# Kernel optimization log

Hardware: AMD Instinct MI355X
Metric: run time of the kernel (lower is better)

Reference implementation:

```python
import jax, jax.numpy as jnp
import numpy as np

# Forest of complete L-ary trees, BFS level-contiguous node numbering.
B_TREES, ARITY, DEPTH = 8, 4, 8
C, M, NGEN = 8, 100, 4
COUNTS = [B_TREES * ARITY**l for l in range(DEPTH + 1)]
OFFS = np.concatenate([[0], np.cumsum(COUNTS)]).astype(np.int64)
DIM = int(OFFS[-1])  # 699048
# tree id of each node: within-level index // (ARITY**level)
BATCH = np.concatenate([np.arange(COUNTS[l]) // (ARITY**l) for l in range(DEPTH + 1)])


def setup_inputs() -> dict:
    key = jax.random.key(0)
    k1, k2, k3, k4 = jax.random.split(key, 4)
    return {
        "x": jax.random.randint(k1, (DIM,), 0, M, dtype=jnp.int32),
        "A": jax.random.normal(k2, (C, C, ARITY, NGEN), dtype=jnp.float32) * 2.5,
        "B_emit": jax.random.normal(k3, (C, M, NGEN), dtype=jnp.float32) * 2.5,
        "Pi": jax.random.normal(k4, (C, NGEN), dtype=jnp.float32) * 2.5,
    }


def _htmm_loglik(x, A, B_emit, Pi):
    # softmax reparameterization (matches F.softmax axes in torch code)
    smA = jax.nn.softmax(A, axis=0)            # [C,C,L,G], over child state
    smA_t = jnp.transpose(smA, (2, 0, 1, 3))   # [L,C,C,G]
    smB = jax.nn.softmax(B_emit, axis=1)       # [C,M,G]
    smPi = jax.nn.softmax(Pi, axis=0)          # [C,G]

    # preliminary downward: prior state distribution per node, level by level.
    # Children of a parent are contiguous with sibling position j = idx % ARITY.
    prior_lvls = [jnp.broadcast_to(smPi, (COUNTS[0], C, NGEN))]
    for l in range(1, DEPTH + 1):
        n_pa = COUNTS[l - 1]
        # prior_child[c] = sum_d A[c, d, pos_j, g] * prior_pa[d]
        pl = jnp.einsum('jcdg,pdg->pjcg', smA_t, prior_lvls[-1])
        prior_lvls.append(pl.reshape(n_pa * ARITY, C, NGEN))
    prior = jnp.concatenate(prior_lvls, axis=0)  # [DIM,C,G]

    em = jnp.transpose(smB[:, x], (1, 0, 2))     # [DIM,C,G]
    beta0 = prior * em

    ll = jnp.zeros((DIM, NGEN), dtype=beta0.dtype)
    # leaves = deepest level
    beta_lvl = beta0[OFFS[DEPTH]:OFFS[DEPTH + 1]]
    nu = beta_lvl.sum(1)                          # [n_leaves,G]
    beta_lvl = beta_lvl / nu[:, None, :]
    ll = ll.at[OFFS[DEPTH]:OFFS[DEPTH + 1]].set(jnp.log(nu))

    # upward recursion, bottom-up
    for l in range(DEPTH, 0, -1):
        n_pa = COUNTS[l - 1]
        ratio = (beta_lvl / prior[OFFS[l]:OFFS[l + 1]]).reshape(n_pa, ARITY, C, NGEN)
        # beta_uv[d] = sum_c A[c, d, pos_j, g] * beta_ch[c] / prior_ch[c]
        beta_uv = jnp.einsum('jcdg,pjcg->pjdg', smA_t, ratio)  # [n_pa,L,C,G]
        beta_pa = beta0[OFFS[l - 1]:OFFS[l]] * jnp.prod(beta_uv, axis=1)
        nu = beta_pa.sum(1)
        beta_lvl = beta_pa / nu[:, None, :]
        ll = ll.at[OFFS[l - 1]:OFFS[l]].set(jnp.log(nu))

    # scatter per-node log-likelihood contributions into per-tree totals
    return jax.ops.segment_sum(ll, jnp.asarray(BATCH), num_segments=B_TREES)  # [B_TREES,G]


def reference(x, A, B_emit, Pi):
    return _htmm_loglik(x, A, B_emit, Pi)
```

## Files before the change

### kernel.cpp

```cpp
#include <hip/hip_runtime.h>

constexpr int OFFS1 = 8, OFFS2 = 40, OFFS3 = 168, OFFS4 = 680;
constexpr int OFFS5 = 2728, OFFS6 = 10920, OFFS7 = 43688, OFFS8 = 174760;


template <int CTRL>
static __device__ __forceinline__ float dppmov(float v) {
  return __int_as_float(__builtin_amdgcn_update_dpp(0, __float_as_int(v), CTRL, 0xF, 0xF, true));
}

static __device__ __forceinline__ float bfly8(float v) {
  v += dppmov<0xB1>(v);
  v += dppmov<0x4E>(v);
  v += dppmov<0x141>(v);
  return v;
}

static __device__ __forceinline__ void oct8(float v, float pv[8]) {
  float m = dppmov<0x141>(v);
  pv[0] = dppmov<0x00>(v); pv[1] = dppmov<0x55>(v);
  pv[2] = dppmov<0xAA>(v); pv[3] = dppmov<0xFF>(v);
  pv[4] = dppmov<0x00>(m); pv[5] = dppmov<0x55>(m);
  pv[6] = dppmov<0xAA>(m); pv[7] = dppmov<0xFF>(m);
}

static __device__ __forceinline__ float dot8(const float w[8], const float v[8]) {
  return w[0]*v[0] + w[1]*v[1] + w[2]*v[2] + w[3]*v[3] +
         w[4]*v[4] + w[5]*v[5] + w[6]*v[6] + w[7]*v[7];
}

static __device__ __forceinline__ void ld8(const float* p, float pv[8]) {
  const float4* q = (const float4*)p;
  float4 a = q[0], b = q[1];
  pv[0] = a.x; pv[1] = a.y; pv[2] = a.z; pv[3] = a.w;
  pv[4] = b.x; pv[5] = b.y; pv[6] = b.z; pv[7] = b.w;
}

static __device__ __forceinline__ void ld8p(const float* p, float wp[8], int h) {
  const float4* q = (const float4*)p;
  float4 a = q[h], b = q[1 - h];
  wp[0] = a.x; wp[1] = a.y; wp[2] = a.z; wp[3] = a.w;
  wp[4] = b.w; wp[5] = b.z; wp[6] = b.y; wp[7] = b.x;
}

static __device__ __forceinline__ float dot8p(const float wp[8], const float* p, int h) {
  const float4* q = (const float4*)p;
  float4 a = q[h], b = q[1 - h];
  return wp[0]*a.x + wp[1]*a.y + wp[2]*a.z + wp[3]*a.w +
         wp[4]*b.w + wp[5]*b.z + wp[6]*b.y + wp[7]*b.x;
}

static __device__ __forceinline__ float rcpf(float x) { return __builtin_amdgcn_rcpf(x); }

static __device__ __forceinline__ float step_down(const float* wtd_l, float v, int j,
                                                  int r, int h) {
  const float* wb = &wtd_l[j * 256 + r];
  float w[8];
#pragma unroll
  for (int k = 0; k < 4; k++) {
    w[k]     = wb[(4 * h + k) * 32];
    w[4 + k] = wb[(7 - 4 * h - k) * 32];
  }
  float pv[8];
  oct8(v, pv);
  return dot8(w, pv);
}

static __device__ __forceinline__ float upprod(const float wup_p[4][8], const float rat[4]) {
  float prod = 1.f;
#pragma unroll
  for (int j = 0; j < 4; j++) {
    float pr[8];
    oct8(rat[j], pr);
    prod *= dot8(wup_p[j], pr);
  }
  return prod;
}

static __device__ __forceinline__ float leaf7(float u7, float e0, float e1, float e2,
                                              float e3, float em, float* acc) {
  float n0 = bfly8(u7 * e0), n1 = bfly8(u7 * e1);
  float n2 = bfly8(u7 * e2), n3 = bfly8(u7 * e3);
  float p01 = n0 * n1, p23 = n2 * n3;
  float prod = (e0 * e1 * rcpf(p01)) * (e2 * e3 * rcpf(p23));
  *acc += __logf(p01) + __logf(p23);
  float nu7 = bfly8(u7 * em * prod);
  *acc += __logf(nu7);
  return em * prod * rcpf(nu7);
}

static __device__ __forceinline__ void build_tables(const float* __restrict__ A,
                                                    const float* __restrict__ Bm,
                                                    const float* __restrict__ Pi,
                                                    float* wtd_l, float* emt_l,
                                                    float* pit_l, float* llb, int t) {
  if (t < 128) {
    int d = t >> 4, j = (t >> 2) & 3, gg = t & 3;
    float v[8], sum = 0.f;
#pragma unroll
    for (int ss = 0; ss < 8; ss++) { v[ss] = __expf(A[((ss * 8 + d) * 4 + j) * 4 + gg]); sum += v[ss]; }
    float inv = rcpf(sum);
#pragma unroll
    for (int ss = 0; ss < 8; ss++) wtd_l[(j * 8 + d) * 32 + gg * 8 + ss] = v[ss] * inv;
  }
  if (t < 4) {
    float v[8], sum = 0.f;
#pragma unroll
    for (int c = 0; c < 8; c++) { v[c] = __expf(Pi[c * 4 + t]); sum += v[c]; }
    float inv = rcpf(sum);
#pragma unroll
    for (int c = 0; c < 8; c++) pit_l[t * 8 + c] = v[c] * inv;
    llb[t] = 0.f;
  }
  {
    int row = t >> 3, part = t & 7, c = row >> 2, gg = row & 3;
    int m0 = part < 4 ? part * 13 : 52 + (part - 4) * 12;
    int mn = part < 4 ? 13 : 12;
    float sum = 0.f;
    for (int m = m0; m < m0 + mn; m++) sum += __expf(Bm[(c * 100 + m) * 4 + gg]);
    sum = bfly8(sum);
    float inv = rcpf(sum);
    for (int m = m0; m < m0 + mn; m++)
      emt_l[m * 32 + gg * 8 + c] = __expf(Bm[(c * 100 + m) * 4 + gg]) * inv;
  }
}

__global__ __launch_bounds__(256) void k_phase1(const int* __restrict__ x,
                                                const float* __restrict__ A,
                                                const float* __restrict__ Bm,
                                                const float* __restrict__ Pi,
                                                float* __restrict__ RAT4,
                                                float* __restrict__ blocksum) {
  __shared__ __align__(16) float wtd_l[1024];
  __shared__ __align__(16) float emt_l[3200];
  __shared__ __align__(16) float pit_l[32];
  __shared__ __align__(16) float rat5buf[16][32];
  __shared__ __align__(16) float pri4buf[4][32];
  __shared__ float llb[4];

  int t = threadIdx.x;
  int r = t & 31, g = r >> 3, s = r & 7, grp = t >> 5;
  int h = s >> 2, gb = g * 8;
  int b = blockIdx.x;

  build_tables(A, Bm, Pi, wtd_l, emt_l, pit_l, llb, t);
  __syncthreads();
  float wtd_p[4][8], wup_p[4][8];
#pragma unroll
  for (int j = 0; j < 4; j++) {
    const float* wb = &wtd_l[j * 256 + r];
#pragma unroll
    for (int k = 0; k < 4; k++) {
      wtd_p[j][k]     = wb[(4 * h + k) * 32];
      wtd_p[j][4 + k] = wb[(7 - 4 * h - k) * 32];
    }
    ld8p(&wtd_l[(j * 8 + s) * 32 + gb], wup_p[j], h);
  }

  float acc = 0.f;
  {
    int n5A = b * 16 + grp, n5B = n5A + 8;
    const int4* x8A = (const int4*)(x + OFFS8 + n5A * 64);
    const int4* x8B = (const int4*)(x + OFFS8 + n5B * 64);
    const int4* x7A = (const int4*)(x + OFFS7 + n5A * 16);
    const int4* x7B = (const int4*)(x + OFFS7 + n5B * 16);
    int4 x6A = *(const int4*)(x + OFFS6 + n5A * 4);
    int4 x6B = *(const int4*)(x + OFFS6 + n5B * 4);
    int x5A = x[OFFS5 + n5A], x5B = x[OFFS5 + n5B];
    const int* x6aA = (const int*)&x6A;
    const int* x6aB = (const int*)&x6B;

    float vA = pit_l[r], vB = vA, pri4A = 0.f, pri4B = 0.f;
#pragma unroll
    for (int k = 1; k <= 5; k++) {
      vA = step_down(wtd_l, vA, (n5A >> (2 * (5 - k))) & 3, r, h);
      vB = step_down(wtd_l, vB, (n5B >> (2 * (5 - k))) & 3, r, h);
      if (k == 4) { pri4A = vA; pri4B = vB; }
    }
    float pv5A[8], pv5B[8];
    oct8(vA, pv5A); oct8(vB, pv5B);

    float rat6A[4], rat6B[4];
#pragma unroll
    for (int q6 = 0; q6 < 4; q6++) {
      float u6A = dot8(wtd_p[q6], pv5A);
      float u6B = dot8(wtd_p[q6], pv5B);
      float pv6A[8], pv6B[8];
      oct8(u6A, pv6A); oct8(u6B, pv6B);
      int4 x7qA = x7A[q6], x7qB = x7B[q6];
      const int* x7aA = (const int*)&x7qA;
      const int* x7aB = (const int*)&x7qB;

      float rat7A[4], rat7B[4];
#pragma unroll
      for (int q7 = 0; q7 < 4; q7++) {
        int4 xlA = x8A[q6 * 4 + q7], xlB = x8B[q6 * 4 + q7];
        const int* xa = (const int*)&xlA;
        const int* xb = (const int*)&xlB;
        float EA[4], EB[4];
#pragma unroll
        for (int j = 0; j < 4; j++) {
          EA[j] = dot8p(wup_p[j], &emt_l[xa[j] * 32 + gb], h);
          EB[j] = dot8p(wup_p[j], &emt_l[xb[j] * 32 + gb], h);
        }
        float u7A = dot8(wtd_p[q7], pv6A);
        float u7B = dot8(wtd_p[q7], pv6B);
        rat7A[q7] = leaf7(u7A, EA[0], EA[1], EA[2], EA[3], emt_l[x7aA[q7] * 32 + r], &acc);
        rat7B[q7] = leaf7(u7B, EB[0], EB[1], EB[2], EB[3], emt_l[x7aB[q7] * 32 + r], &acc);
      }
      float prod6A = upprod(wup_p, rat7A);
      float prod6B = upprod(wup_p, rat7B);
      float em6A = emt_l[x6aA[q6] * 32 + r];
      float em6B = emt_l[x6aB[q6] * 32 + r];
      float nu6A = bfly8(u6A * em6A * prod6A);
      float nu6B = bfly8(u6B * em6B * prod6B);
      acc += __logf(nu6A) + __logf(nu6B);
      rat6A[q6] = em6A * prod6A * rcpf(nu6A);
      rat6B[q6] = em6B * prod6B * rcpf(nu6B);
    }
    float prod5A = upprod(wup_p, rat6A);
    float prod5B = upprod(wup_p, rat6B);
    float em5A = emt_l[x5A * 32 + r], em5B = emt_l[x5B * 32 + r];
    float nu5A = bfly8(vA * em5A * prod5A);
    float nu5B = bfly8(vB * em5B * prod5B);
    acc += __logf(nu5A) + __logf(nu5B);
    rat5buf[grp][r] = em5A * prod5A * rcpf(nu5A);
    rat5buf[8 + grp][r] = em5B * prod5B * rcpf(nu5B);
    if ((grp & 3) == 0) {
      pri4buf[grp >> 2][r] = pri4A;
      pri4buf[2 + (grp >> 2)][r] = pri4B;
    }
  }
  __syncthreads();

  if (grp < 4) {
    int n4 = b * 4 + grp;
    float prod = 1.f;
#pragma unroll
    for (int j = 0; j < 4; j++) prod *= dot8p(wup_p[j], &rat5buf[grp * 4 + j][gb], h);
    float em = emt_l[x[OFFS4 + n4] * 32 + r];
    float pr4 = pri4buf[grp][r];
    float nu = bfly8(pr4 * em * prod);
    acc += __logf(nu);
    RAT4[n4 * 32 + r] = em * prod * rcpf(nu);
  }

  if (s == 0) atomicAdd(&llb[g], acc);
  __syncthreads();
  if (t < 4) blocksum[b * 4 + t] = llb[t];
}

__global__ __launch_bounds__(256) void k_phase2(const int* __restrict__ x,
                                                const float* __restrict__ A,
                                                const float* __restrict__ Bm,
                                                const float* __restrict__ Pi,
                                                const float* __restrict__ RAT4,
                                                const float* __restrict__ blocksum,
                                                float* __restrict__ out) {
  __shared__ __align__(16) float wtd_l[1024];
  __shared__ __align__(16) float emt_l[3200];
  __shared__ __align__(16) float pit_l[32];
  __shared__ __align__(16) float stg[8192];
  __shared__ __align__(16) float xb[640];
  __shared__ float llb[4];

  int t = threadIdx.x;
  int r = t & 31, g = r >> 3, s = r & 7, grp = t >> 5;
  int h = s >> 2, gb = g * 8;
  int tree = blockIdx.x;

  build_tables(A, Bm, Pi, wtd_l, emt_l, pit_l, llb, t);
  {
    const float4* src = (const float4*)(RAT4 + tree * 8192);
    float4* dst = (float4*)stg;
#pragma unroll
    for (int i = 0; i < 8; i++) dst[i * 256 + t] = src[i * 256 + t];
  }
  __syncthreads();

  float wtd_p[4][8], wup_p[4][8];
#pragma unroll
  for (int j = 0; j < 4; j++) {
    const float* wb = &wtd_l[j * 256 + r];
#pragma unroll
    for (int k = 0; k < 4; k++) {
      wtd_p[j][k]     = wb[(4 * h + k) * 32];
      wtd_p[j][4 + k] = wb[(7 - 4 * h - k) * 32];
    }
    ld8p(&wtd_l[(j * 8 + s) * 32 + gb], wup_p[j], h);
  }

  float acc2 = 0.f;
  {
    int n2A = tree * 16 + grp, n2B = n2A + 8;
    int4 x3A = *(const int4*)(x + OFFS3 + n2A * 4);
    int4 x3B = *(const int4*)(x + OFFS3 + n2B * 4);
    int x2A = x[OFFS2 + n2A], x2B = x[OFFS2 + n2B];
    const int* xa = (const int*)&x3A;
    const int* xbv = (const int*)&x3B;
    float v2A = pit_l[r], v2B = v2A;
    v2A = step_down(wtd_l, v2A, (n2A >> 2) & 3, r, h);
    v2B = step_down(wtd_l, v2B, (n2B >> 2) & 3, r, h);
    v2A = step_down(wtd_l, v2A, n2A & 3, r, h);
    v2B = step_down(wtd_l, v2B, n2B & 3, r, h);
    float pv2A[8], pv2B[8];
    oct8(v2A, pv2A); oct8(v2B, pv2B);
    float rat3A[4], rat3B[4];
#pragma unroll
    for (int j3 = 0; j3 < 4; j3++) {
      int i3A = grp * 4 + j3, i3B = (8 + grp) * 4 + j3;
      float p3A = dot8(wtd_p[j3], pv2A);
      float p3B = dot8(wtd_p[j3], pv2B);
      float prodA = 1.f, prodB = 1.f;
#pragma unroll
      for (int j = 0; j < 4; j++) {
        prodA *= dot8p(wup_p[j], &stg[(i3A * 4 + j) * 32 + gb], h);
        prodB *= dot8p(wup_p[j], &stg[(i3B * 4 + j) * 32 + gb], h);
      }
      float emA = emt_l[xa[j3] * 32 + r], emB = emt_l[xbv[j3] * 32 + r];
      float nuA = bfly8(p3A * emA * prodA), nuB = bfly8(p3B * emB * prodB);
      acc2 += __logf(nuA) + __logf(nuB);
      rat3A[j3] = emA * prodA * rcpf(nuA);
      rat3B[j3] = emB * prodB * rcpf(nuB);
    }
    float prodA = upprod(wup_p, rat3A);
    float prodB = upprod(wup_p, rat3B);
    float emA = emt_l[x2A * 32 + r], emB = emt_l[x2B * 32 + r];
    float nuA = bfly8(v2A * emA * prodA), nuB = bfly8(v2B * emB * prodB);
    acc2 += __logf(nuA) + __logf(nuB);
    xb[grp * 32 + r] = emA * prodA * rcpf(nuA);
    xb[(8 + grp) * 32 + r] = emB * prodB * rcpf(nuB);
  }
  __syncthreads();
  if (grp < 4) {
    int n1g = tree * 4 + grp;
    float v1 = step_down(wtd_l, pit_l[r], grp, r, h);
    float prod = 1.f;
#pragma unroll
    for (int j = 0; j < 4; j++) prod *= dot8p(wup_p[j], &xb[(grp * 4 + j) * 32 + gb], h);
    float em = emt_l[x[OFFS1 + n1g] * 32 + r];
    float nu = bfly8(v1 * em * prod);
    acc2 += __logf(nu);
    xb[512 + grp * 32 + r] = em * prod * rcpf(nu);
  }
  __syncthreads();
  if (grp == 0) {
    float pr = pit_l[r];
    float prod = 1.f;
#pragma unroll
    for (int j = 0; j < 4; j++) prod *= dot8p(wup_p[j], &xb[512 + j * 32 + gb], h);
    float em = emt_l[x[tree] * 32 + r];
    float nu = bfly8(pr * em * prod);
    acc2 += __logf(nu);
  }
  __syncthreads();
  if (s == 0) atomicAdd(&llb[g], acc2);
  float v = blocksum[tree * 256 + t];
  __syncthreads();
  stg[t] = v;
  __syncthreads();
#pragma unroll
  for (int off = 128; off >= 4; off >>= 1) {
    if (t < off) stg[t] += stg[t + off];
    __syncthreads();
  }
  if (t < 4) out[tree * 4 + t] = stg[t] + llb[t];
}

extern "C" void kernel_launch(void* const* d_in, const int* in_sizes, int n_in,
                              void* d_out, int out_size, void* d_ws, size_t ws_size,
                              hipStream_t stream) {
  const int* x = (const int*)d_in[0];
  const float* A = (const float*)d_in[1];
  const float* Bm = (const float*)d_in[2];
  const float* Pi = (const float*)d_in[3];
  float* ws = (float*)d_ws;
  float* blocksum = ws + 256;
  float* RAT4 = ws + 256 + 2048;
  float* out = (float*)d_out;

  k_phase1<<<512, 256, 0, stream>>>(x, A, Bm, Pi, RAT4, blocksum);
  k_phase2<<<8, 256, 0, stream>>>(x, A, Bm, Pi, RAT4, blocksum, out);
}
```

Baseline: 94.66 us.

## Halve per-block work, double grid, and use transposed padded down-weights in LDS

Each warp-group now processes one level-5 subtree instead of two, so phase 1 launches twice as many blocks. The per-thread wtd_p register array is dropped; a padded transposed copy of the down-weights (wtdT) is built in LDS and read with float2 loads. Launch bounds request two blocks per CU. The aim is lower register pressure and more waves in flight, paid for by rebuilding the softmax tables in twice as many blocks and by extra LDS reads. Phase 2 now sums two blocksum entries per thread to match the doubled grid.

Result: slower. 100.1 us (+5.8%).

```diff
diff --git a/kernel.cpp b/kernel.cpp
--- a/kernel.cpp
+++ b/kernel.cpp
@@ -29,13 +29,6 @@
          w[4]*v[4] + w[5]*v[5] + w[6]*v[6] + w[7]*v[7];
 }
 
-static __device__ __forceinline__ void ld8(const float* p, float pv[8]) {
-  const float4* q = (const float4*)p;
-  float4 a = q[0], b = q[1];
-  pv[0] = a.x; pv[1] = a.y; pv[2] = a.z; pv[3] = a.w;
-  pv[4] = b.x; pv[5] = b.y; pv[6] = b.z; pv[7] = b.w;
-}
-
 static __device__ __forceinline__ void ld8p(const float* p, float wp[8], int h) {
   const float4* q = (const float4*)p;
   float4 a = q[h], b = q[1 - h];
@@ -50,7 +43,21 @@
          wp[4]*b.w + wp[5]*b.z + wp[6]*b.y + wp[7]*b.x;
 }
 
+static __device__ __forceinline__ float dot8pT(const float wp[8], const float* row, int h) {
+  const float2* q = (const float2*)row;
+  float2 a = q[2 * h], b = q[2 * h + 1], c = q[3 - 2 * h], d = q[2 - 2 * h];
+  return wp[0]*a.x + wp[1]*a.y + wp[2]*b.x + wp[3]*b.y +
+         wp[4]*c.y + wp[5]*c.x + wp[6]*d.y + wp[7]*d.x;
+}
+
 static __device__ __forceinline__ float rcpf(float x) { return __builtin_amdgcn_rcpf(x); }
+
+static __device__ __forceinline__ float step_downT(const float* wtdT, float v, int j,
+                                                   int sg, int h) {
+  float pv[8];
+  oct8(v, pv);
+  return dot8pT(pv, &wtdT[(j * 32 + sg) * 10], h);
+}
 
 static __device__ __forceinline__ float step_down(const float* wtd_l, float v, int j,
                                                   int r, int h) {
@@ -125,121 +132,97 @@
   }
 }
 
-__global__ __launch_bounds__(256) void k_phase1(const int* __restrict__ x,
-                                                const float* __restrict__ A,
-                                                const float* __restrict__ Bm,
-                                                const float* __restrict__ Pi,
-                                                float* __restrict__ RAT4,
-                                                float* __restrict__ blocksum) {
+__global__ __launch_bounds__(256, 2) void k_phase1(const int* __restrict__ x,
+                                                   const float* __restrict__ A,
+                                                   const float* __restrict__ Bm,
+                                                   const float* __restrict__ Pi,
+                                                   float* __restrict__ RAT4,
+                                                   float* __restrict__ blocksum) {
   __shared__ __align__(16) float wtd_l[1024];
+  __shared__ __align__(16) float wtdT[1280];
   __shared__ __align__(16) float emt_l[3200];
   __shared__ __align__(16) float pit_l[32];
-  __shared__ __align__(16) float rat5buf[16][32];
-  __shared__ __align__(16) float pri4buf[4][32];
+  __shared__ __align__(16) float xb[320];
   __shared__ float llb[4];
 
   int t = threadIdx.x;
   int r = t & 31, g = r >> 3, s = r & 7, grp = t >> 5;
   int h = s >> 2, gb = g * 8;
+  int sg = s * 4 + g;
   int b = blockIdx.x;
 
   build_tables(A, Bm, Pi, wtd_l, emt_l, pit_l, llb, t);
   __syncthreads();
-  float wtd_p[4][8], wup_p[4][8];
-#pragma unroll
-  for (int j = 0; j < 4; j++) {
-    const float* wb = &wtd_l[j * 256 + r];
-#pragma unroll
-    for (int k = 0; k < 4; k++) {
-      wtd_p[j][k]     = wb[(4 * h + k) * 32];
-      wtd_p[j][4 + k] = wb[(7 - 4 * h - k) * 32];
-    }
-    ld8p(&wtd_l[(j * 8 + s) * 32 + gb], wup_p[j], h);
-  }
+  if (t < 128) {
+    int j = t >> 5, ss = (t >> 2) & 7, gg = t & 3;
+#pragma unroll
+    for (int d = 0; d < 8; d++) wtdT[t * 10 + d] = wtd_l[(j * 8 + d) * 32 + gg * 8 + ss];
+  }
+  float wup_p[4][8];
+#pragma unroll
+  for (int j = 0; j < 4; j++) ld8p(&wtd_l[(j * 8 + s) * 32 + gb], wup_p[j], h);
+  __syncthreads();
 
   float acc = 0.f;
   {
-    int n5A = b * 16 + grp, n5B = n5A + 8;
-    const int4* x8A = (const int4*)(x + OFFS8 + n5A * 64);
-    const int4* x8B = (const int4*)(x + OFFS8 + n5B * 64);
-    const int4* x7A = (const int4*)(x + OFFS7 + n5A * 16);
-    const int4* x7B = (const int4*)(x + OFFS7 + n5B * 16);
-    int4 x6A = *(const int4*)(x + OFFS6 + n5A * 4);
-    int4 x6B = *(const int4*)(x + OFFS6 + n5B * 4);
-    int x5A = x[OFFS5 + n5A], x5B = x[OFFS5 + n5B];
-    const int* x6aA = (const int*)&x6A;
-    const int* x6aB = (const int*)&x6B;
-
-    float vA = pit_l[r], vB = vA, pri4A = 0.f, pri4B = 0.f;
+    int n5 = b * 8 + grp;
+    const int4* x8v = (const int4*)(x + OFFS8 + n5 * 64);
+    const int4* x7p = (const int4*)(x + OFFS7 + n5 * 16);
+    int4 x6v = *(const int4*)(x + OFFS6 + n5 * 4);
+    int x5s = x[OFFS5 + n5];
+    const int* x6a = (const int*)&x6v;
+
+    float v5 = pit_l[r], pri4 = 0.f;
 #pragma unroll
     for (int k = 1; k <= 5; k++) {
-      vA = step_down(wtd_l, vA, (n5A >> (2 * (5 - k))) & 3, r, h);
-      vB = step_down(wtd_l, vB, (n5B >> (2 * (5 - k))) & 3, r, h);
-      if (k == 4) { pri4A = vA; pri4B = vB; }
+      v5 = step_downT(wtdT, v5, (n5 >> (2 * (5 - k))) & 3, sg, h);
+      if (k == 4) pri4 = v5;
     }
-    float pv5A[8], pv5B[8];
-    oct8(vA, pv5A); oct8(vB, pv5B);
-
-    float rat6A[4], rat6B[4];
+    float pv5[8];
+    oct8(v5, pv5);
+
+    float rat6[4];
 #pragma unroll
     for (int q6 = 0; q6 < 4; q6++) {
-      float u6A = dot8(wtd_p[q6], pv5A);
-      float u6B = dot8(wtd_p[q6], pv5B);
-      float pv6A[8], pv6B[8];
-      oct8(u6A, pv6A); oct8(u6B, pv6B);
-      int4 x7qA = x7A[q6], x7qB = x7B[q6];
-      const int* x7aA = (const int*)&x7qA;
-      const int* x7aB = (const int*)&x7qB;
-
-      float rat7A[4], rat7B[4];
+      float u6 = dot8pT(pv5, &wtdT[(q6 * 32 + sg) * 10], h);
+      float pv6[8];
+      oct8(u6, pv6);
+      int4 x7q = x7p[q6];
+      const int* x7a = (const int*)&x7q;
+
+      float rat7[4];
 #pragma unroll
       for (int q7 = 0; q7 < 4; q7++) {
-        int4 xlA = x8A[q6 * 4 + q7], xlB = x8B[q6 * 4 + q7];
-        const int* xa = (const int*)&xlA;
-        const int* xb = (const int*)&xlB;
-        float EA[4], EB[4];
-#pragma unroll
-        for (int j = 0; j < 4; j++) {
-          EA[j] = dot8p(wup_p[j], &emt_l[xa[j] * 32 + gb], h);
-          EB[j] = dot8p(wup_p[j], &emt_l[xb[j] * 32 + gb], h);
-        }
-        float u7A = dot8(wtd_p[q7], pv6A);
-        float u7B = dot8(wtd_p[q7], pv6B);
-        rat7A[q7] = leaf7(u7A, EA[0], EA[1], EA[2], EA[3], emt_l[x7aA[q7] * 32 + r], &acc);
-        rat7B[q7] = leaf7(u7B, EB[0], EB[1], EB[2], EB[3], emt_l[x7aB[q7] * 32 + r], &acc);
+        int4 xl = x8v[q6 * 4 + q7];
+        const int* xa = (const int*)&xl;
+        float E[4];
+#pragma unroll
+        for (int j = 0; j < 4; j++) E[j] = dot8p(wup_p[j], &emt_l[xa[j] * 32 + gb], h);
+        float u7 = dot8pT(pv6, &wtdT[(q7 * 32 + sg) * 10], h);
+        rat7[q7] = leaf7(u7, E[0], E[1], E[2], E[3], emt_l[x7a[q7] * 32 + r], &acc);
       }
-      float prod6A = upprod(wup_p, rat7A);
-      float prod6B = upprod(wup_p, rat7B);
-      float em6A = emt_l[x6aA[q6] * 32 + r];
-      float em6B = emt_l[x6aB[q6] * 32 + r];
-      float nu6A = bfly8(u6A * em6A * prod6A);
-      float nu6B = bfly8(u6B * em6B * prod6B);
-      acc += __logf(nu6A) + __logf(nu6B);
-      rat6A[q6] = em6A * prod6A * rcpf(nu6A);
-      rat6B[q6] = em6B * prod6B * rcpf(nu6B);
+      float prod6 = upprod(wup_p, rat7);
+      float em6 = emt_l[x6a[q6] * 32 + r];
+      float nu6 = bfly8(u6 * em6 * prod6);
+      acc += __logf(nu6);
+      rat6[q6] = em6 * prod6 * rcpf(nu6);
     }
-    float prod5A = upprod(wup_p, rat6A);
-    float prod5B = upprod(wup_p, rat6B);
-    float em5A = emt_l[x5A * 32 + r], em5B = emt_l[x5B * 32 + r];
-    float nu5A = bfly8(vA * em5A * prod5A);
-    float nu5B = bfly8(vB * em5B * prod5B);
-    acc += __logf(nu5A) + __logf(nu5B);
-    rat5buf[grp][r] = em5A * prod5A * rcpf(nu5A);
-    rat5buf[8 + grp][r] = em5B * prod5B * rcpf(nu5B);
-    if ((grp & 3) == 0) {
-      pri4buf[grp >> 2][r] = pri4A;
-      pri4buf[2 + (grp >> 2)][r] = pri4B;
-    }
-  }
-  __syncthreads();
-
-  if (grp < 4) {
-    int n4 = b * 4 + grp;
+    float prod5 = upprod(wup_p, rat6);
+    float em5 = emt_l[x5s * 32 + r];
+    float nu5 = bfly8(v5 * em5 * prod5);
+    acc += __logf(nu5);
+    xb[grp * 32 + r] = em5 * prod5 * rcpf(nu5);
+    if ((grp & 3) == 0) xb[256 + (grp >> 2) * 32 + r] = pri4;
+  }
+  __syncthreads();
+
+  if (grp < 2) {
+    int n4 = b * 2 + grp;
     float prod = 1.f;
 #pragma unroll
-    for (int j = 0; j < 4; j++) prod *= dot8p(wup_p[j], &rat5buf[grp * 4 + j][gb], h);
+    for (int j = 0; j < 4; j++) prod *= dot8p(wup_p[j], &xb[(grp * 4 + j) * 32 + gb], h);
     float em = emt_l[x[OFFS4 + n4] * 32 + r];
-    float pr4 = pri4buf[grp][r];
+    float pr4 = xb[256 + grp * 32 + r];
     float nu = bfly8(pr4 * em * prod);
     acc += __logf(nu);
     RAT4[n4 * 32 + r] = em * prod * rcpf(nu);
@@ -355,7 +338,7 @@
   }
   __syncthreads();
   if (s == 0) atomicAdd(&llb[g], acc2);
-  float v = blocksum[tree * 256 + t];
+  float v = blocksum[tree * 512 + t] + blocksum[tree * 512 + 256 + t];
   __syncthreads();
   stg[t] = v;
   __syncthreads();
@@ -376,9 +359,9 @@
   const float* Pi = (const float*)d_in[3];
   float* ws = (float*)d_ws;
   float* blocksum = ws + 256;
-  float* RAT4 = ws + 256 + 2048;
+  float* RAT4 = ws + 256 + 4096;
   float* out = (float*)d_out;
 
-  k_phase1<<<512, 256, 0, stream>>>(x, A, Bm, Pi, RAT4, blocksum);
+  k_phase1<<<1024, 256, 0, stream>>>(x, A, Bm, Pi, RAT4, blocksum);
   k_phase2<<<8, 256, 0, stream>>>(x, A, Bm, Pi, RAT4, blocksum, out);
 }
```
